# Optimization experiments

Measured on AMD Instinct MI355X. Metric: run time of the kernel, lower is better.

The kernel has to match this reference:

```python
import jax, jax.numpy as jnp
import numpy as np

DIM = 1024
DIM_QK = 1024
DIM_V = 1024
H = 16
SCALE = 1.0 / (DIM_QK ** 0.5)  # NOTE: module scales by sqrt(dim_qk), not sqrt(head_dim)


def setup_inputs() -> dict:
    key = jax.random.key(0)
    ks = jax.random.split(key, 12)
    B, S = 2, 2048
    q = jax.random.normal(ks[0], (B, S, DIM), jnp.float32)
    k = jax.random.normal(ks[1], (B, S, DIM), jnp.float32)
    v = jax.random.normal(ks[2], (B, S, DIM), jnp.float32)
    mask = jax.random.randint(ks[3], (B, 1, S, S), 0, 2) > 0  # True = masked
    s = 1.0 / np.sqrt(DIM)
    Wq = jax.random.uniform(ks[4], (DIM_QK, DIM), jnp.float32, -s, s)
    bq = jax.random.uniform(ks[5], (DIM_QK,), jnp.float32, -s, s)
    Wk = jax.random.uniform(ks[6], (DIM_QK, DIM), jnp.float32, -s, s)
    bk = jax.random.uniform(ks[7], (DIM_QK,), jnp.float32, -s, s)
    Wv = jax.random.uniform(ks[8], (DIM_V, DIM), jnp.float32, -s, s)
    bv = jax.random.uniform(ks[9], (DIM_V,), jnp.float32, -s, s)
    Wo = jax.random.uniform(ks[10], (DIM_V, DIM), jnp.float32, -s, s)
    bo = jax.random.uniform(ks[11], (DIM_V,), jnp.float32, -s, s)
    return {"q": q, "k": k, "v": v, "mask": mask,
            "Wq": Wq, "bq": bq, "Wk": Wk, "bk": bk,
            "Wv": Wv, "bv": bv, "Wo": Wo, "bo": bo}


def reference(q, k, v, mask, Wq, bq, Wk, bk, Wv, bv, Wo, bo):
    B, Sq, _ = q.shape
    Skv = k.shape[1]
    # projections (torch Linear: x @ W.T + b)
    qh = (q @ Wq.T + bq).reshape(B, Sq, H, DIM_QK // H).transpose(0, 2, 1, 3)   # [B,H,Sq,dk]
    kh = (k @ Wk.T + bk).reshape(B, Skv, H, DIM_QK // H).transpose(0, 2, 1, 3)  # [B,H,Skv,dk]
    vh = (v @ Wv.T + bv).reshape(B, Skv, H, DIM_V // H).transpose(0, 2, 1, 3)   # [B,H,Skv,dv]
    attn = jnp.einsum('bhqd,bhkd->bhqk', qh, kh) * SCALE
    attn = jnp.where(mask, jnp.float32(-1e20), attn)
    attn = jax.nn.softmax(attn, axis=-1)
    # dropout is identity in eval / p=0
    out = jnp.einsum('bhqk,bhkd->bhqd', attn, vh)            # [B,H,Sq,dv]
    out = out.transpose(0, 2, 1, 3).reshape(B, Sq, DIM_V)
    return out @ Wo.T + bo
```

## Files before the change

### kernel.cpp

```cpp
#include <hip/hip_runtime.h>
#include <hip/hip_bf16.h>

typedef __attribute__((ext_vector_type(8))) __bf16 bf16x8;
typedef __attribute__((ext_vector_type(4))) short short4v;
typedef __attribute__((ext_vector_type(4))) float f32x4;
typedef __attribute__((ext_vector_type(4))) unsigned int uint4v;
typedef __attribute__((ext_vector_type(2))) unsigned int uint2v;

#define S_LEN 2048
#define DIM_  1024
#define HDIM  64
#define SCALE2 0.045084441f

#define EXP2F(x) __builtin_amdgcn_exp2f(x)

#define ATTN_SWZ(row, col8) (((row) * 64) + (((col8) ^ ((row) & 7)) << 3))

__device__ __forceinline__ void async_copy16(const void* gp, void* lp) {
  __builtin_amdgcn_global_load_lds(
      (const __attribute__((address_space(1))) unsigned int*)gp,
      (__attribute__((address_space(3))) unsigned int*)lp, 16, 0, 0);
}

__device__ __forceinline__ unsigned f2bf_u(float f) {
  unsigned u = __builtin_bit_cast(unsigned, f);
  return (u + 0x7FFFu + ((u >> 16) & 1u)) >> 16;
}
__device__ __forceinline__ unsigned pack2(float a, float b) {
  return f2bf_u(a) | (f2bf_u(b) << 16);
}
__device__ __forceinline__ unsigned pack2f(float a, float b) {
  unsigned ua = __builtin_bit_cast(unsigned, a) + 0x8000u;
  unsigned ub = __builtin_bit_cast(unsigned, b) + 0x8000u;
  return __builtin_amdgcn_perm(ub, ua, 0x07060302u);
}

__global__ __launch_bounds__(256) void cvt_kernel(
    const float* __restrict__ s0, const float* __restrict__ s1, const float* __restrict__ s2,
    const float* __restrict__ s3, const float* __restrict__ s4, const float* __restrict__ s5,
    const float* __restrict__ s6,
    __hip_bfloat16* __restrict__ d0, __hip_bfloat16* __restrict__ d1, __hip_bfloat16* __restrict__ d2,
    __hip_bfloat16* __restrict__ d3, __hip_bfloat16* __restrict__ d4, __hip_bfloat16* __restrict__ d5,
    __hip_bfloat16* __restrict__ d6)
{
  const float* srcs[7] = {s0, s1, s2, s3, s4, s5, s6};
  __hip_bfloat16* dsts[7] = {d0, d1, d2, d3, d4, d5, d6};
  const int sizes[7] = {4194304, 4194304, 4194304, 1048576, 1048576, 1048576, 1048576};
  int rg = blockIdx.y;
  int base = (blockIdx.x * 256 + threadIdx.x) * 8;
  if (base >= sizes[rg]) return;
  const float* s = srcs[rg] + base;
  f32x4 a = *(const f32x4*)s;
  f32x4 b = *(const f32x4*)(s + 4);
  uint4v o;
  o.x = pack2(a[0], a[1]); o.y = pack2(a[2], a[3]);
  o.z = pack2(b[0], b[1]); o.w = pack2(b[2], b[3]);
  *(uint4v*)(dsts[rg] + base) = o;
}

__global__ __launch_bounds__(256) void maskbits_kernel(
    const int* __restrict__ mask, unsigned long long* __restrict__ bits)
{
  int w = (blockIdx.x * 256 + threadIdx.x) >> 6;
  int lane = threadIdx.x & 63;
  int m = mask[(size_t)w * 64 + lane];
  unsigned long long bal = __ballot(m != 0);
  if (lane == 0) bits[w] = bal;
}

__device__ __forceinline__ void swz(int r, int& m0, int& n0) {
  int g  = r >> 6;
  int yy = (r >> 3) & 7;
  int xl = r & 7;
  m0 = (g * 8 + xl) * 128;
  n0 = yy * 128;
}

__global__ __launch_bounds__(256) void qkv_gemm_kernel(
    const __hip_bfloat16* __restrict__ xq, const __hip_bfloat16* __restrict__ xk,
    const __hip_bfloat16* __restrict__ xv,
    const __hip_bfloat16* __restrict__ Wq, const float* __restrict__ bq,
    const __hip_bfloat16* __restrict__ Wk, const float* __restrict__ bk,
    const __hip_bfloat16* __restrict__ Wv, const float* __restrict__ bv,
    __hip_bfloat16* __restrict__ Q, __hip_bfloat16* __restrict__ Kk,
    __hip_bfloat16* __restrict__ VT)
{
  const __hip_bfloat16 *X, *W; const float* bias;
  if (blockIdx.z == 0)      { X = xq; W = Wq; bias = bq; }
  else if (blockIdx.z == 1) { X = xk; W = Wk; bias = bk; }
  else                      { X = xv; W = Wv; bias = bv; }

  constexpr int K = 1024, N = 1024;
  __shared__ alignas(16) __hip_bfloat16 As[2][128 * 32];
  __shared__ alignas(16) __hip_bfloat16 Bs[2][128 * 32];
  const int tid  = threadIdx.x;
  const int lane = tid & 63;
  const int wave = tid >> 6;
  const int t    = lane & 15;
  const int quad = lane >> 4;
  const int wm   = wave >> 1;
  const int wn   = wave & 1;
  int m0, n0;
  swz(blockIdx.x, m0, n0);

  f32x4 acc[4][4] = {};

  const int c0 = tid, c1 = 256 + tid;
  const int r0 = c0 >> 2, o0 = (c0 & 3) * 8;
  const int r1 = c1 >> 2, o1 = (c1 & 3) * 8;
  const __hip_bfloat16* xp0 = &X[(size_t)(m0 + r0) * K + o0];
  const __hip_bfloat16* xp1 = &X[(size_t)(m0 + r1) * K + o1];
  const __hip_bfloat16* wp0 = &W[(size_t)(n0 + r0) * K + o0];
  const __hip_bfloat16* wp1 = &W[(size_t)(n0 + r1) * K + o1];

  async_copy16(xp0, &As[0][c0 * 8]);
  async_copy16(xp1, &As[0][c1 * 8]);
  async_copy16(wp0, &Bs[0][c0 * 8]);
  async_copy16(wp1, &Bs[0][c1 * 8]);

  int buf = 0;
  for (int k0 = 0; k0 < K; k0 += 32) {
    __syncthreads();
    if (k0 + 32 < K) {
      int nb = buf ^ 1;
      int kn = k0 + 32;
      async_copy16(xp0 + kn, &As[nb][c0 * 8]);
      async_copy16(xp1 + kn, &As[nb][c1 * 8]);
      async_copy16(wp0 + kn, &Bs[nb][c0 * 8]);
      async_copy16(wp1 + kn, &Bs[nb][c1 * 8]);
    }
    bf16x8 a[4], b[4];
#pragma unroll
    for (int i = 0; i < 4; ++i)
      a[i] = *(const bf16x8*)&As[buf][(wm * 64 + i * 16 + t) * 32 + quad * 8];
#pragma unroll
    for (int j = 0; j < 4; ++j)
      b[j] = *(const bf16x8*)&Bs[buf][(wn * 64 + j * 16 + t) * 32 + quad * 8];
#pragma unroll
    for (int i = 0; i < 4; ++i)
#pragma unroll
      for (int j = 0; j < 4; ++j)
        acc[i][j] = __builtin_amdgcn_mfma_f32_16x16x32_bf16(a[i], b[j], acc[i][j], 0, 0, 0);
    buf ^= 1;
  }

  float bj[4];
#pragma unroll
  for (int j = 0; j < 4; ++j)
    bj[j] = bias[n0 + wn * 64 + j * 16 + t];

  if (blockIdx.z == 2) {
#pragma unroll
    for (int i = 0; i < 4; ++i)
#pragma unroll
      for (int j = 0; j < 4; ++j) {
        int m = m0 + wm * 64 + i * 16 + quad * 4;
        int n = n0 + wn * 64 + j * 16 + t;
        int bb = m >> 11, kv = m & 2047;
        int hh = n >> 6,  dv = n & 63;
        uint2v o;
        o.x = pack2(acc[i][j][0] + bj[j], acc[i][j][1] + bj[j]);
        o.y = pack2(acc[i][j][2] + bj[j], acc[i][j][3] + bj[j]);
        *(uint2v*)&VT[(size_t)(((bb * 16 + hh) * 64) + dv) * 2048 + kv] = o;
      }
  } else {
    const bool isq = (blockIdx.z == 0);
    __hip_bfloat16* Out = isq ? Q : Kk;
    const float sc = isq ? SCALE2 : 1.0f;
#pragma unroll
    for (int i = 0; i < 4; ++i)
#pragma unroll
      for (int j = 0; j < 4; ++j)
#pragma unroll
        for (int r = 0; r < 4; ++r) {
          int m = m0 + wm * 64 + i * 16 + quad * 4 + r;
          int n = n0 + wn * 64 + j * 16 + t;
          Out[(size_t)m * N + n] = __float2bfloat16((acc[i][j][r] + bj[j]) * sc);
        }
  }
}

__global__ __launch_bounds__(256) void proj_gemm_kernel(
    const __hip_bfloat16* __restrict__ X, const __hip_bfloat16* __restrict__ W,
    const float* __restrict__ bias, float* __restrict__ Out)
{
  constexpr int K = 1024, N = 1024;
  __shared__ alignas(16) __hip_bfloat16 As[2][128 * 32];
  __shared__ alignas(16) __hip_bfloat16 Bs[2][128 * 32];
  const int tid  = threadIdx.x;
  const int lane = tid & 63;
  const int wave = tid >> 6;
  const int t    = lane & 15;
  const int quad = lane >> 4;
  const int wm   = wave >> 1;
  const int wn   = wave & 1;
  int m0, n0;
  swz(blockIdx.x, m0, n0);

  f32x4 acc[4][4] = {};

  const int c0 = tid, c1 = 256 + tid;
  const int r0 = c0 >> 2, o0 = (c0 & 3) * 8;
  const int r1 = c1 >> 2, o1 = (c1 & 3) * 8;
  const __hip_bfloat16* xp0 = &X[(size_t)(m0 + r0) * K + o0];
  const __hip_bfloat16* xp1 = &X[(size_t)(m0 + r1) * K + o1];
  const __hip_bfloat16* wp0 = &W[(size_t)(n0 + r0) * K + o0];
  const __hip_bfloat16* wp1 = &W[(size_t)(n0 + r1) * K + o1];

  async_copy16(xp0, &As[0][c0 * 8]);
  async_copy16(xp1, &As[0][c1 * 8]);
  async_copy16(wp0, &Bs[0][c0 * 8]);
  async_copy16(wp1, &Bs[0][c1 * 8]);

  int buf = 0;
  for (int k0 = 0; k0 < K; k0 += 32) {
    __syncthreads();
    if (k0 + 32 < K) {
      int nb = buf ^ 1;
      int kn = k0 + 32;
      async_copy16(xp0 + kn, &As[nb][c0 * 8]);
      async_copy16(xp1 + kn, &As[nb][c1 * 8]);
      async_copy16(wp0 + kn, &Bs[nb][c0 * 8]);
      async_copy16(wp1 + kn, &Bs[nb][c1 * 8]);
    }
    bf16x8 a[4], b[4];
#pragma unroll
    for (int i = 0; i < 4; ++i)
      a[i] = *(const bf16x8*)&As[buf][(wm * 64 + i * 16 + t) * 32 + quad * 8];
#pragma unroll
    for (int j = 0; j < 4; ++j)
      b[j] = *(const bf16x8*)&Bs[buf][(wn * 64 + j * 16 + t) * 32 + quad * 8];
#pragma unroll
    for (int i = 0; i < 4; ++i)
#pragma unroll
      for (int j = 0; j < 4; ++j)
        acc[i][j] = __builtin_amdgcn_mfma_f32_16x16x32_bf16(a[i], b[j], acc[i][j], 0, 0, 0);
    buf ^= 1;
  }

  float bj[4];
#pragma unroll
  for (int j = 0; j < 4; ++j)
    bj[j] = bias[n0 + wn * 64 + j * 16 + t];
#pragma unroll
  for (int i = 0; i < 4; ++i)
#pragma unroll
    for (int j = 0; j < 4; ++j)
#pragma unroll
      for (int r = 0; r < 4; ++r) {
        int m = m0 + wm * 64 + i * 16 + quad * 4 + r;
        int n = n0 + wn * 64 + j * 16 + t;
        Out[(size_t)m * N + n] = acc[i][j][r] + bj[j];
      }
}

__global__ __launch_bounds__(256) void attn_kernel(
    const __hip_bfloat16* __restrict__ Qb,
    const __hip_bfloat16* __restrict__ Kb,
    const __hip_bfloat16* __restrict__ VT,
    const unsigned long long* __restrict__ mbits,
    __hip_bfloat16* __restrict__ Ob)
{
  const int bid = blockIdx.x;
  const int qt = bid & 31;
  const int h  = (bid >> 5) & 15;
  const int b  = bid >> 9;
  const int qb = qt * 64;

  __shared__ alignas(16) __hip_bfloat16 Qs[64 * 64];
  __shared__ alignas(16) __hip_bfloat16 Ks[2][64 * 64];
  __shared__ alignas(16) __hip_bfloat16 Vt[2][64 * 64];

  const int tid  = threadIdx.x;
  const int lane = tid & 63;
  const int wave = tid >> 6;
  const int t    = lane & 15;
  const int quad = lane >> 4;

  const int r0 = tid >> 3;
  const int r1 = 32 + r0;
  const int k0c = ((tid & 7) ^ (r0 & 7)) << 3;
  const int k1c = ((tid & 7) ^ (r1 & 7)) << 3;
  const __hip_bfloat16* kp0 = &Kb[((size_t)(b * S_LEN + r0)) * DIM_ + h * HDIM + k0c];
  const __hip_bfloat16* kp1 = &Kb[((size_t)(b * S_LEN + r1)) * DIM_ + h * HDIM + k1c];
  const size_t vtbase = (size_t)((b * 16 + h) * 64) * 2048;
  const __hip_bfloat16* vp0 = &VT[vtbase + (size_t)r0 * 2048 + k0c];
  const __hip_bfloat16* vp1 = &VT[vtbase + (size_t)r1 * 2048 + k1c];

  async_copy16(kp0, &Ks[0][tid * 8]);
  async_copy16(kp1, &Ks[0][(256 + tid) * 8]);
  async_copy16(vp0, &Vt[0][tid * 8]);
  async_copy16(vp1, &Vt[0][(256 + tid) * 8]);

#pragma unroll
  for (int r = 0; r < 2; ++r) {
    int c = r * 256 + tid;
    int row = c >> 3, c8 = c & 7;
    uint4 raw = *(const uint4*)&Qb[((size_t)(b * S_LEN + qb + row)) * DIM_ + h * HDIM + c8 * 8];
    *(uint4*)&Qs[ATTN_SWZ(row, c8)] = raw;
  }
  __syncthreads();

  bf16x8 qf[2];
#pragma unroll
  for (int ks = 0; ks < 2; ++ks)
    qf[ks] = *(const bf16x8*)&Qs[ATTN_SWZ(wave * 16 + t, ks * 4 + quad)];

  f32x4 lp4 = {0.f, 0.f, 0.f, 0.f};
  f32x4 o[4] = {};

  const int qg = qb + wave * 16 + t;
  const size_t mbase = ((size_t)b * S_LEN + qg) * 32;

  int buf = 0;
  for (int kvt = 0; kvt < 32; ++kvt) {
    unsigned long long mw = mbits[mbase + kvt];
    if (kvt) __syncthreads();
    if (kvt + 1 < 32) {
      int nb = buf ^ 1;
      size_t koff = (size_t)(kvt + 1) * 64 * DIM_;
      int    voff = (kvt + 1) * 64;
      async_copy16(kp0 + koff, &Ks[nb][tid * 8]);
      async_copy16(kp1 + koff, &Ks[nb][(256 + tid) * 8]);
      async_copy16(vp0 + voff, &Vt[nb][tid * 8]);
      async_copy16(vp1 + voff, &Vt[nb][(256 + tid) * 8]);
    }

    __builtin_amdgcn_s_setprio(1);
    float e[4][4];
#pragma unroll
    for (int i = 0; i < 4; ++i) {
      f32x4 z = {};
      bf16x8 a0 = *(const bf16x8*)&Ks[buf][ATTN_SWZ(i * 16 + t, quad)];
      z = __builtin_amdgcn_mfma_f32_16x16x32_bf16(a0, qf[0], z, 0, 0, 0);
      bf16x8 a1 = *(const bf16x8*)&Ks[buf][ATTN_SWZ(i * 16 + t, 4 + quad)];
      z = __builtin_amdgcn_mfma_f32_16x16x32_bf16(a1, qf[1], z, 0, 0, 0);
      unsigned mq = (unsigned)((mw >> (i * 16 + quad * 4)) & 0xFull);
#pragma unroll
      for (int r = 0; r < 4; ++r) {
        float v = ((mq >> r) & 1u) ? -1e20f : z[r];
        float ex = EXP2F(v);
        e[i][r] = ex;
        lp4[r] += ex;
      }
    }

    short4v pf[4];
#pragma unroll
    for (int j = 0; j < 4; ++j) {
      uint2v pk;
      pk.x = pack2f(e[j][0], e[j][1]);
      pk.y = pack2f(e[j][2], e[j][3]);
      pf[j] = __builtin_bit_cast(short4v, pk);
    }

#pragma unroll
    for (int j = 0; j < 4; ++j)
#pragma unroll
      for (int n = 0; n < 4; ++n) {
        short4v va = *(const short4v*)&Vt[buf][(n * 16 + t) * 64 +
                         (((j * 2 + (quad >> 1)) ^ (t & 7)) << 3) + (quad & 1) * 4];
        o[n] = __builtin_amdgcn_mfma_f32_16x16x16bf16_1k(va, pf[j], o[n], 0, 0, 0);
      }
    __builtin_amdgcn_s_setprio(0);
    buf ^= 1;
  }

  float lp = (lp4[0] + lp4[1]) + (lp4[2] + lp4[3]);
  lp += __shfl_xor(lp, 16, 64);
  lp += __shfl_xor(lp, 32, 64);
  float rl = 1.0f / lp;

  __hip_bfloat16* Ts = Qs;
  __syncthreads();
#pragma unroll
  for (int n = 0; n < 4; ++n) {
    uint2v pk;
    pk.x = pack2f(o[n][0] * rl, o[n][1] * rl);
    pk.y = pack2f(o[n][2] * rl, o[n][3] * rl);
    *(uint2v*)&Ts[(wave * 16 + t) * 64 +
                  (((n * 2 + (quad >> 1)) ^ (t & 7)) << 3) + (quad & 1) * 4] = pk;
  }
  __syncthreads();
  {
    int row = tid >> 2;
    int b0  = (tid & 3) * 2;
    uint4 x0 = *(const uint4*)&Ts[row * 64 + ((b0 ^ (row & 7)) << 3)];
    uint4 x1 = *(const uint4*)&Ts[row * 64 + (((b0 + 1) ^ (row & 7)) << 3)];
    int d0 = (tid & 3) * 16;
    __hip_bfloat16* dst = &Ob[((size_t)(b * S_LEN + qb + row)) * DIM_ + h * HDIM + d0];
    *(uint4*)dst = x0;
    *(uint4*)(dst + 8) = x1;
  }
}

extern "C" void kernel_launch(void* const* d_in, const int* in_sizes, int n_in,
                              void* d_out, int out_size, void* d_ws, size_t ws_size,
                              hipStream_t stream) {
  const float* q  = (const float*)d_in[0];
  const float* k  = (const float*)d_in[1];
  const float* v  = (const float*)d_in[2];
  const int*   mk = (const int*)d_in[3];
  const float* Wq = (const float*)d_in[4];
  const float* bq = (const float*)d_in[5];
  const float* Wk = (const float*)d_in[6];
  const float* bk = (const float*)d_in[7];
  const float* Wv = (const float*)d_in[8];
  const float* bv = (const float*)d_in[9];
  const float* Wo = (const float*)d_in[10];
  const float* bo = (const float*)d_in[11];
  float* out = (float*)d_out;

  char* ws = (char*)d_ws;
  const size_t MB = 1024 * 1024;
  __hip_bfloat16* Qb  = (__hip_bfloat16*)(ws);
  __hip_bfloat16* Kb  = (__hip_bfloat16*)(ws + 8  * MB);
  __hip_bfloat16* VTb = (__hip_bfloat16*)(ws + 16 * MB);
  __hip_bfloat16* Ob  = (__hip_bfloat16*)(ws + 24 * MB);
  __hip_bfloat16* xqb = (__hip_bfloat16*)(ws + 32 * MB);
  __hip_bfloat16* xkb = (__hip_bfloat16*)(ws + 40 * MB);
  __hip_bfloat16* xvb = (__hip_bfloat16*)(ws + 48 * MB);
  __hip_bfloat16* Wqb = (__hip_bfloat16*)(ws + 56 * MB);
  __hip_bfloat16* Wkb = (__hip_bfloat16*)(ws + 58 * MB);
  __hip_bfloat16* Wvb = (__hip_bfloat16*)(ws + 60 * MB);
  __hip_bfloat16* Wob = (__hip_bfloat16*)(ws + 62 * MB);
  unsigned long long* mbits = (unsigned long long*)(ws + 64 * MB);

  cvt_kernel<<<dim3(2048, 7), 256, 0, stream>>>(q, k, v, Wq, Wk, Wv, Wo,
                                                xqb, xkb, xvb, Wqb, Wkb, Wvb, Wob);
  maskbits_kernel<<<dim3(32768), 256, 0, stream>>>(mk, mbits);
  qkv_gemm_kernel<<<dim3(256, 1, 3), 256, 0, stream>>>(xqb, xkb, xvb,
                                                       Wqb, bq, Wkb, bk, Wvb, bv,
                                                       Qb, Kb, VTb);
  attn_kernel<<<dim3(1024), 256, 0, stream>>>(Qb, Kb, VTb, mbits, Ob);
  proj_gemm_kernel<<<dim3(256), 256, 0, stream>>>(Ob, Wob, bo, out);
}
```

Before: 274.0 us.

## Fuse mask packing into convert kernel, remap block order, use hardware bf16 pack

Folds the mask-to-bitmask kernel into the conversion kernel as an extra grid row, saving one launch, with each wave now packing 16 mask words. It also remaps the GEMM tile order and the attention block index so consecutive blocks are spread across XCD-like groups, aiming at better L2 locality. The custom truncation-style bf16 pack is replaced with __float22bfloat162_rn, which may lower to a native packed convert instruction but may cost more if it does not.

```diff
diff --git a/kernel.cpp b/kernel.cpp
--- a/kernel.cpp
+++ b/kernel.cpp
@@ -29,10 +29,12 @@
 __device__ __forceinline__ unsigned pack2(float a, float b) {
   return f2bf_u(a) | (f2bf_u(b) << 16);
 }
-__device__ __forceinline__ unsigned pack2f(float a, float b) {
-  unsigned ua = __builtin_bit_cast(unsigned, a) + 0x8000u;
-  unsigned ub = __builtin_bit_cast(unsigned, b) + 0x8000u;
-  return __builtin_amdgcn_perm(ub, ua, 0x07060302u);
+__device__ __forceinline__ unsigned cvtpk(float a, float b) {
+  float2 f; f.x = a; f.y = b;
+  __hip_bfloat162 h = __float22bfloat162_rn(f);
+  unsigned u;
+  __builtin_memcpy(&u, &h, 4);
+  return u;
 }
 
 __global__ __launch_bounds__(256) void cvt_kernel(
@@ -41,8 +43,21 @@
     const float* __restrict__ s6,
     __hip_bfloat16* __restrict__ d0, __hip_bfloat16* __restrict__ d1, __hip_bfloat16* __restrict__ d2,
     __hip_bfloat16* __restrict__ d3, __hip_bfloat16* __restrict__ d4, __hip_bfloat16* __restrict__ d5,
-    __hip_bfloat16* __restrict__ d6)
+    __hip_bfloat16* __restrict__ d6,
+    const int* __restrict__ mask, unsigned long long* __restrict__ bits)
 {
+  if (blockIdx.y == 7) {
+    int wave = threadIdx.x >> 6, lane = threadIdx.x & 63;
+    int gw = blockIdx.x * 4 + wave;
+#pragma unroll
+    for (int it = 0; it < 16; ++it) {
+      int w = gw * 16 + it;
+      int m = mask[(size_t)w * 64 + lane];
+      unsigned long long bal = __ballot(m != 0);
+      if (lane == 0) bits[w] = bal;
+    }
+    return;
+  }
   const float* srcs[7] = {s0, s1, s2, s3, s4, s5, s6};
   __hip_bfloat16* dsts[7] = {d0, d1, d2, d3, d4, d5, d6};
   const int sizes[7] = {4194304, 4194304, 4194304, 1048576, 1048576, 1048576, 1048576};
@@ -58,22 +73,11 @@
   *(uint4v*)(dsts[rg] + base) = o;
 }
 
-__global__ __launch_bounds__(256) void maskbits_kernel(
-    const int* __restrict__ mask, unsigned long long* __restrict__ bits)
-{
-  int w = (blockIdx.x * 256 + threadIdx.x) >> 6;
-  int lane = threadIdx.x & 63;
-  int m = mask[(size_t)w * 64 + lane];
-  unsigned long long bal = __ballot(m != 0);
-  if (lane == 0) bits[w] = bal;
-}
-
 __device__ __forceinline__ void swz(int r, int& m0, int& n0) {
-  int g  = r >> 6;
-  int yy = (r >> 3) & 7;
-  int xl = r & 7;
-  m0 = (g * 8 + xl) * 128;
-  n0 = yy * 128;
+  int c  = ((r & 7) << 2) | (r >> 6);
+  int xl = (r >> 3) & 7;
+  m0 = ((c >> 3) * 8 + xl) * 128;
+  n0 = (c & 7) * 128;
 }
 
 __global__ __launch_bounds__(256) void qkv_gemm_kernel(
@@ -262,9 +266,10 @@
     __hip_bfloat16* __restrict__ Ob)
 {
   const int bid = blockIdx.x;
-  const int qt = bid & 31;
-  const int h  = (bid >> 5) & 15;
-  const int b  = bid >> 9;
+  const int qt = (bid >> 3) & 31;
+  const int g  = ((bid & 7) << 2) | (bid >> 8);
+  const int h  = g & 15;
+  const int b  = g >> 4;
   const int qb = qt * 64;
 
   __shared__ alignas(16) __hip_bfloat16 Qs[64 * 64];
@@ -349,8 +354,8 @@
 #pragma unroll
     for (int j = 0; j < 4; ++j) {
       uint2v pk;
-      pk.x = pack2f(e[j][0], e[j][1]);
-      pk.y = pack2f(e[j][2], e[j][3]);
+      pk.x = cvtpk(e[j][0], e[j][1]);
+      pk.y = cvtpk(e[j][2], e[j][3]);
       pf[j] = __builtin_bit_cast(short4v, pk);
     }
 
@@ -376,8 +381,8 @@
 #pragma unroll
   for (int n = 0; n < 4; ++n) {
     uint2v pk;
-    pk.x = pack2f(o[n][0] * rl, o[n][1] * rl);
-    pk.y = pack2f(o[n][2] * rl, o[n][3] * rl);
+    pk.x = cvtpk(o[n][0] * rl, o[n][1] * rl);
+    pk.y = cvtpk(o[n][2] * rl, o[n][3] * rl);
     *(uint2v*)&Ts[(wave * 16 + t) * 64 +
                   (((n * 2 + (quad >> 1)) ^ (t & 7)) << 3) + (quad & 1) * 4] = pk;
   }
@@ -426,9 +431,9 @@
   __hip_bfloat16* Wob = (__hip_bfloat16*)(ws + 62 * MB);
   unsigned long long* mbits = (unsigned long long*)(ws + 64 * MB);
 
-  cvt_kernel<<<dim3(2048, 7), 256, 0, stream>>>(q, k, v, Wq, Wk, Wv, Wo,
-                                                xqb, xkb, xvb, Wqb, Wkb, Wvb, Wob);
-  maskbits_kernel<<<dim3(32768), 256, 0, stream>>>(mk, mbits);
+  cvt_kernel<<<dim3(2048, 8), 256, 0, stream>>>(q, k, v, Wq, Wk, Wv, Wo,
+                                                xqb, xkb, xvb, Wqb, Wkb, Wvb, Wob,
+                                                mk, mbits);
   qkv_gemm_kernel<<<dim3(256, 1, 3), 256, 0, stream>>>(xqb, xkb, xvb,
                                                        Wqb, bq, Wkb, bk, Wvb, bv,
                                                        Qb, Kb, VTb);
```

Measured after the change: 268.9 us. No clear change (-1.8%).
